# Kernel optimization log

Hardware: AMD Instinct MI355X
Metric: run time of the kernel (lower is better)

The kernel has to match this reference:

```python
import jax, jax.numpy as jnp
import numpy as np

NUM_HEADS = 16
THETA = 10000.0


def setup_inputs() -> dict:
    key = jax.random.key(0)
    k1, k2, k3, k4 = jax.random.split(key, 4)
    B, T, D = 2, 2048, 1024
    x = jax.random.normal(k1, (B, T, D), dtype=jnp.float32)
    token_positions = jnp.sort(
        jax.random.randint(k2, (B, T), 0, 2048), axis=-1
    ).astype(jnp.int32)
    sigma_qkv = float(np.sqrt(2.0 / (D + 3 * D)))
    sigma_out = float(np.sqrt(2.0 / (D + D)))
    W_qkv = jax.random.normal(k3, (3 * D, D), dtype=jnp.float32) * sigma_qkv
    W_out = jax.random.normal(k4, (D, D), dtype=jnp.float32) * sigma_out
    return {"x": x, "token_positions": token_positions, "W_qkv": W_qkv, "W_out": W_out}


def _apply_rope(t, cos, sin):
    # t: [B, H, T, d_k]; cos/sin: [B, T, d_k//2]
    B, H, T, dk = t.shape
    t2 = t.reshape(B, H, T, dk // 2, 2)
    te, to = t2[..., 0], t2[..., 1]
    c = cos[:, None]  # [B, 1, T, dk//2]
    s = sin[:, None]
    ye = te * c - to * s
    yo = to * c + te * s
    return jnp.stack([ye, yo], axis=-1).reshape(B, H, T, dk)


def reference(x, token_positions, W_qkv, W_out):
    B, T, D = x.shape
    H = NUM_HEADS
    dk = D // H

    # fused QKV projection: [B, T, 3D] -> split (three, h, d) on last dim
    qkv = jnp.einsum("btd,od->bto", x, W_qkv).reshape(B, T, 3, H, dk)
    qkv = jnp.transpose(qkv, (2, 0, 3, 1, 4))  # [3, B, H, T, dk]
    q, k, v = qkv[0], qkv[1], qkv[2]

    # RoPE angles from token positions
    n = jnp.arange(dk // 2, dtype=jnp.float32)
    inv_freq = THETA ** (-2.0 * n / dk)  # [dk//2]
    angles = token_positions.astype(jnp.float32)[..., None] * inv_freq  # [B, T, dk//2]
    cos, sin = jnp.cos(angles), jnp.sin(angles)
    q = _apply_rope(q, cos, sin)
    k = _apply_rope(k, cos, sin)

    # causal scaled dot-product attention
    scores = jnp.einsum("bhid,bhjd->bhij", q, k) / jnp.sqrt(jnp.float32(dk))
    causal = jnp.tril(jnp.ones((T, T), dtype=bool))
    scores = jnp.where(causal, scores, -jnp.inf)
    probs = jax.nn.softmax(scores, axis=-1)
    attn = jnp.einsum("bhij,bhjd->bhid", probs, v)  # [B, H, T, dk]

    concat = jnp.transpose(attn, (0, 2, 1, 3)).reshape(B, T, D)
    return jnp.einsum("btd,od->bto", concat, W_out)
```

## Files before the change

kernel.cpp:

```cpp
#include <hip/hip_runtime.h>
#include <hip/hip_bf16.h>
#include <cmath>

#define T_SEQ 2048
#define D_MODEL 1024
#define NHEAD 16
#define DK 64

typedef short bf16x8 __attribute__((ext_vector_type(8)));
typedef float f32x4 __attribute__((ext_vector_type(4)));
typedef float f32x16 __attribute__((ext_vector_type(16)));
typedef unsigned uint2v __attribute__((ext_vector_type(2)));

union U8 { unsigned u[4]; bf16x8 v; };

#define VMCNT(n) asm volatile("s_waitcnt vmcnt(" #n ")" ::: "memory")
#define BAR() __builtin_amdgcn_s_barrier()
#define SFENCE() __builtin_amdgcn_sched_barrier(0)

__device__ __forceinline__ short f2b(float f) {
    unsigned u = __builtin_bit_cast(unsigned, f);
    unsigned r = (u + 0x7FFFu + ((u >> 16) & 1u)) >> 16;
    return (short)r;
}

__device__ __forceinline__ void gll16(const void* g, void* l) {
    __builtin_amdgcn_global_load_lds(
        (__attribute__((address_space(1))) void*)g,
        (__attribute__((address_space(3))) void*)l, 16, 0, 0);
}

__device__ __forceinline__ bf16x8 lds_frag(const short* base, int row, int chunk) {
    return *reinterpret_cast<const bf16x8*>(
        (const char*)base + row * 128 + ((chunk * 16) ^ ((row & 7) << 4)));
}

__device__ __forceinline__ unsigned pkbf16(float a, float b) {
    unsigned r;
    asm("v_cvt_pk_bf16_f32 %0, %1, %2" : "=v"(r) : "v"(a), "v"(b));
    return r;
}
__device__ __forceinline__ void pl32swap(unsigned& a, unsigned& b) {
    uint2v r = __builtin_amdgcn_permlane32_swap(a, b, false, false);
    a = r.x; b = r.y;
}

__global__ __launch_bounds__(256) void cvt_all(const float* __restrict__ x,
                                               const float* __restrict__ wq,
                                               const float* __restrict__ wo,
                                               const int* __restrict__ pos,
                                               short* __restrict__ xb,
                                               short* __restrict__ wqb,
                                               short* __restrict__ wob,
                                               float* __restrict__ ct,
                                               float* __restrict__ st) {
    int i = blockIdx.x * 256 + threadIdx.x;
    if (i >= 1048576) {
        int j = i - 1048576;
        int bt = j >> 5, n = j & 31;
        float p = (float)pos[bt];
        float invf = expf((float)n * (-2.0f / (float)DK) * 9.210340371976184f);
        float s, c;
        sincosf(p * invf, &s, &c);
        ct[j] = c; st[j] = s;
        return;
    }
    const float* src;
    short* dst;
    int srcoff, c;
    if (i < 524288) {
        c = i;
        int tile = c >> 9, cc = c & 511;
        int kblk = cc >> 7, row = cc & 127;
        int rb = tile >> 5, kb = tile & 31;
        srcoff = (rb * 128 + row) * D_MODEL + kb * 32 + kblk * 8;
        src = x; dst = xb;
    } else if (i < 917504) {
        c = i - 524288;
        int tile = c >> 9, cc = c & 511;
        int kblk = cc >> 7, row = cc & 127;
        int rb = tile >> 5, kb = tile & 31;
        srcoff = (rb * 128 + row) * D_MODEL + kb * 32 + kblk * 8;
        src = wq; dst = wqb;
    } else {
        c = i - 917504;
        int tile = c >> 8, cc = c & 255;
        int kblk = cc >> 6, row = cc & 63;
        int nb = tile >> 5, kb = tile & 31;
        srcoff = (nb * 64 + row) * D_MODEL + kb * 32 + kblk * 8;
        src = wo; dst = wob;
    }
    float4 a = *reinterpret_cast<const float4*>(src + srcoff);
    float4 b = *reinterpret_cast<const float4*>(src + srcoff + 4);
    bf16x8 v;
    v[0] = f2b(a.x); v[1] = f2b(a.y); v[2] = f2b(a.z); v[3] = f2b(a.w);
    v[4] = f2b(b.x); v[5] = f2b(b.y); v[6] = f2b(b.z); v[7] = f2b(b.w);
    reinterpret_cast<bf16x8*>(dst)[c] = v;
}

__global__ __launch_bounds__(256, 3) void gemm_qkv(const short* __restrict__ xb,
                                                   const short* __restrict__ wb,
                                                   const float* __restrict__ ct,
                                                   const float* __restrict__ st,
                                                   short* __restrict__ Qo,
                                                   short* __restrict__ Ko,
                                                   short* __restrict__ Vt) {
    __shared__ short SM[3][8192];
    const int tid = threadIdx.x;
    const int w = tid >> 6, l = tid & 63, lg = l >> 4, li = l & 15;
    const int wr = w >> 1, wc = w & 1;
    const int bn = blockIdx.x * 128, bm = blockIdx.y * 128;

    const short* pA = xb + (size_t)blockIdx.y * 32 * 4096 + (w * 128 + l) * 8;
    const short* pB = wb + (size_t)blockIdx.x * 32 * 4096 + (w * 128 + l) * 8;

    f32x4 zero = {0.f, 0.f, 0.f, 0.f};
    f32x4 acc[4][4];
#pragma unroll
    for (int m = 0; m < 4; ++m)
#pragma unroll
        for (int n = 0; n < 4; ++n) acc[m][n] = zero;

#define GSTAGE(buf, t_)                                               \
    do {                                                              \
        const size_t ko = (size_t)(t_) * 4096;                        \
        gll16(pA + ko,       &SM[buf][w * 1024]);                     \
        gll16(pA + ko + 512, &SM[buf][w * 1024 + 512]);               \
        gll16(pB + ko,       &SM[buf][4096 + w * 1024]);              \
        gll16(pB + ko + 512, &SM[buf][4096 + w * 1024 + 512]);        \
    } while (0)

    GSTAGE(0, 0);
    GSTAGE(1, 1);

    for (int t = 0; t < 32; ++t) {
        if (t < 31) { VMCNT(4); } else { VMCNT(0); }
        BAR();
        SFENCE();
        if (t + 2 < 32) GSTAGE((t + 2) % 3, t + 2);
        const short* Ac = &SM[t % 3][0];
        const short* Bc = &SM[t % 3][4096];
        bf16x8 a[4], b[4];
#pragma unroll
        for (int m = 0; m < 4; ++m)
            a[m] = *reinterpret_cast<const bf16x8*>(&Ac[lg * 1024 + (wr * 64 + m * 16 + li) * 8]);
#pragma unroll
        for (int n = 0; n < 4; ++n)
            b[n] = *reinterpret_cast<const bf16x8*>(&Bc[lg * 1024 + (wc * 64 + n * 16 + li) * 8]);
        __builtin_amdgcn_s_setprio(1);
#pragma unroll
        for (int m = 0; m < 4; ++m)
#pragma unroll
            for (int n = 0; n < 4; ++n)
                acc[m][n] = __builtin_amdgcn_mfma_f32_16x16x32_bf16(a[m], b[n], acc[m][n], 0, 0, 0);
        __builtin_amdgcn_s_setprio(0);
    }
#undef GSTAGE

    const int which = bn >> 10;
    const int h = ((bn >> 6) + wc) & 15;
    if (which == 2) {
        __syncthreads();
        short* scr = &SM[0][0] + w * 4096;
#pragma unroll
        for (int n = 0; n < 4; ++n)
#pragma unroll
            for (int m = 0; m < 4; ++m)
#pragma unroll
                for (int rp = 0; rp < 2; ++rp) {
                    int d = n * 16 + li;
                    int t64 = m * 16 + lg * 4 + rp * 2;
                    unsigned pk = pkbf16(acc[m][n][rp * 2], acc[m][n][rp * 2 + 1]);
                    *reinterpret_cast<unsigned*>(
                        (char*)scr + ((d * 128 + t64 * 2) ^ ((d & 7) << 4))) = pk;
                }
        const int mi0 = bm + wr * 64;
        const int b0 = mi0 >> 11, t0 = mi0 & (T_SEQ - 1);
        short* vbase = Vt + (size_t)(b0 * NHEAD + h) * DK * T_SEQ + t0;
#pragma unroll
        for (int db = 0; db < 8; ++db) {
            int d = db * 8 + (l >> 3);
            int ch = l & 7;
            bf16x8 v = *reinterpret_cast<const bf16x8*>(
                (char*)scr + ((d * 128 + ch * 16) ^ ((d & 7) << 4)));
            *reinterpret_cast<bf16x8*>(vbase + (size_t)d * T_SEQ + ch * 8) = v;
        }
    } else {
#pragma unroll
        for (int n = 0; n < 4; ++n) {
            const int d = n * 16 + li;
#pragma unroll
            for (int m = 0; m < 4; ++m)
#pragma unroll
                for (int r = 0; r < 4; ++r) {
                    const int mi = bm + wr * 64 + m * 16 + lg * 4 + r;
                    const int b_ = mi >> 11, tt = mi & (T_SEQ - 1);
                    float v = acc[m][n][r];
                    float vp = __shfl_xor(v, 1);
                    int nn = n * 8 + (li >> 1);
                    float c = ct[(size_t)mi * 32 + nn];
                    float s = st[(size_t)mi * 32 + nn];
                    float o = (d & 1) ? (v * c + vp * s) : (v * c - vp * s);
                    if (which == 0) o *= 0.18033688011112042f;
                    short* dst = (which == 0) ? Qo : Ko;
                    dst[((size_t)((b_ * NHEAD + h) * T_SEQ + tt)) * DK + d] = f2b(o);
                }
        }
    }
}

__global__ __launch_bounds__(128, 2) void attn(const short* __restrict__ Q,
                                               const short* __restrict__ K,
                                               const short* __restrict__ Vt,
                                               short* __restrict__ Cc) {
    __shared__ short Kls[2][4096];
    __shared__ short Vls[2][4096];

    const int bid = blockIdx.x;
    const int bh = bid & 31;
    const int qt = 31 - (bid >> 5);
    const int ntb = qt + 1;

    const int tid = threadIdx.x;
    const int w = tid >> 6, l = tid & 63;
    const int l31 = l & 31, hi = l >> 5, hi4 = hi * 4, hi8 = hi * 8;
    const int q0w = qt * 64 + w * 32;

    const short* Qh = Q + (size_t)bh * T_SEQ * DK;
    const short* Kh = K + (size_t)bh * T_SEQ * DK;
    const short* Vh = Vt + (size_t)bh * DK * T_SEQ;

    bf16x8 qf[4];
#pragma unroll
    for (int ks = 0; ks < 4; ++ks)
        qf[ks] = *reinterpret_cast<const bf16x8*>(&Qh[(size_t)(q0w + l31) * DK + ks * 16 + hi8]);

    f32x16 o0 = {0.f,0.f,0.f,0.f,0.f,0.f,0.f,0.f,0.f,0.f,0.f,0.f,0.f,0.f,0.f,0.f};
    f32x16 o1 = o0;
    float m = -3.0e38f;
    float lsum = 0.f;

    int rr[4], cb[4];
#pragma unroll
    for (int j = 0; j < 4; ++j) {
        int c = j * 128 + tid;
        rr[j] = c >> 3;
        cb[j] = ((c & 7) ^ (rr[j] & 7)) * 8;
    }

    auto astage = [&](int buf, int n0_) {
#pragma unroll
        for (int j = 0; j < 4; ++j)
            gll16(Kh + (size_t)(n0_ + rr[j]) * DK + cb[j], &Kls[buf][j * 1024 + w * 512]);
#pragma unroll
        for (int j = 0; j < 4; ++j)
            gll16(Vh + (size_t)rr[j] * T_SEQ + n0_ + cb[j], &Vls[buf][j * 1024 + w * 512]);
    };

    astage(0, 0);

    for (int t = 0; t < ntb; ++t) {
        VMCNT(0);
        BAR();
        SFENCE();
        if (t + 1 < ntb) astage((t + 1) & 1, (t + 1) * 64);
        const int n0 = t * 64;
        const short* Kc = Kls[t & 1];
        const short* Vc = Vls[t & 1];

        f32x16 s0 = {0.f,0.f,0.f,0.f,0.f,0.f,0.f,0.f,0.f,0.f,0.f,0.f,0.f,0.f,0.f,0.f};
        f32x16 s1 = s0;
        __builtin_amdgcn_s_setprio(1);
#pragma unroll
        for (int ks = 0; ks < 4; ++ks) {
            bf16x8 kf0 = lds_frag(Kc, l31,      ks * 2 + hi);
            bf16x8 kf1 = lds_frag(Kc, 32 + l31, ks * 2 + hi);
            s0 = __builtin_amdgcn_mfma_f32_32x32x16_bf16(kf0, qf[ks], s0, 0, 0, 0);
            s1 = __builtin_amdgcn_mfma_f32_32x32x16_bf16(kf1, qf[ks], s1, 0, 0, 0);
        }
        __builtin_amdgcn_s_setprio(0);

        float p[32];
#pragma unroll
        for (int r = 0; r < 16; ++r) { p[r] = s0[r]; p[16 + r] = s1[r]; }

        if (n0 + 64 > q0w) {
            const int qrel = q0w + l31 - n0;
#pragma unroll
            for (int r = 0; r < 16; ++r) {
                const int kvm = (r & 3) + 8 * (r >> 2) + hi4;
                if (kvm > qrel) p[r] = -3.0e38f;
                if (kvm + 32 > qrel) p[16 + r] = -3.0e38f;
            }
        }

        float t16[16];
#pragma unroll
        for (int r = 0; r < 16; ++r) t16[r] = fmaxf(p[r], p[16 + r]);
#pragma unroll
        for (int d = 8; d >= 1; d >>= 1)
#pragma unroll
            for (int r = 0; r < 8; ++r)
                if (r < d) t16[r] = fmaxf(t16[r], t16[r + d]);
        float tmax = fmaxf(t16[0], __shfl_xor(t16[0], 32));

        if (__any(tmax > m + 8.0f)) {
            float mnew = fmaxf(m, tmax);
            float alpha = __builtin_amdgcn_exp2f(m - mnew);
            m = mnew;
#pragma unroll
            for (int r = 0; r < 16; ++r) {
                float ar = __shfl(alpha, (r & 3) + 8 * (r >> 2) + hi4);
                o0[r] *= ar; o1[r] *= ar;
            }
            lsum *= alpha;
        }

#pragma unroll
        for (int r = 0; r < 32; ++r) p[r] = __builtin_amdgcn_exp2f(p[r] - m);
        float a16[16];
#pragma unroll
        for (int r = 0; r < 16; ++r) a16[r] = p[r] + p[16 + r];
#pragma unroll
        for (int d = 8; d >= 1; d >>= 1)
#pragma unroll
            for (int r = 0; r < 8; ++r)
                if (r < d) a16[r] += a16[r + d];
        lsum += a16[0] + __shfl_xor(a16[0], 32);

        __builtin_amdgcn_s_setprio(1);
#pragma unroll
        for (int kb = 0; kb < 2; ++kb) {
            unsigned pk0 = pkbf16(p[kb * 16 + 0],  p[kb * 16 + 1]);
            unsigned pk1 = pkbf16(p[kb * 16 + 2],  p[kb * 16 + 3]);
            unsigned pk2 = pkbf16(p[kb * 16 + 4],  p[kb * 16 + 5]);
            unsigned pk3 = pkbf16(p[kb * 16 + 6],  p[kb * 16 + 7]);
            unsigned pk4 = pkbf16(p[kb * 16 + 8],  p[kb * 16 + 9]);
            unsigned pk5 = pkbf16(p[kb * 16 + 10], p[kb * 16 + 11]);
            unsigned pk6 = pkbf16(p[kb * 16 + 12], p[kb * 16 + 13]);
            unsigned pk7 = pkbf16(p[kb * 16 + 14], p[kb * 16 + 15]);
            pl32swap(pk0, pk2); pl32swap(pk1, pk3);
            pl32swap(pk4, pk6); pl32swap(pk5, pk7);
            U8 f0, f1;
            f0.u[0] = pk0; f0.u[1] = pk1; f0.u[2] = pk2; f0.u[3] = pk3;
            f1.u[0] = pk4; f1.u[1] = pk5; f1.u[2] = pk6; f1.u[3] = pk7;
            bf16x8 v00 = lds_frag(Vc, l31,      kb * 4 + hi);
            bf16x8 v01 = lds_frag(Vc, l31,      kb * 4 + 2 + hi);
            bf16x8 v10 = lds_frag(Vc, 32 + l31, kb * 4 + hi);
            bf16x8 v11 = lds_frag(Vc, 32 + l31, kb * 4 + 2 + hi);
            o0 = __builtin_amdgcn_mfma_f32_32x32x16_bf16(f0.v, v00, o0, 0, 0, 0);
            o0 = __builtin_amdgcn_mfma_f32_32x32x16_bf16(f1.v, v01, o0, 0, 0, 0);
            o1 = __builtin_amdgcn_mfma_f32_32x32x16_bf16(f0.v, v10, o1, 0, 0, 0);
            o1 = __builtin_amdgcn_mfma_f32_32x32x16_bf16(f1.v, v11, o1, 0, 0, 0);
        }
        __builtin_amdgcn_s_setprio(0);
    }

    const int b = bh >> 4, h = bh & 15;
    const float linv = 1.0f / lsum;
#pragma unroll
    for (int r = 0; r < 16; ++r) {
        const int qoff = (r & 3) + 8 * (r >> 2) + hi4;
        float inv = __shfl(linv, qoff);
        const int mg = b * T_SEQ + q0w + qoff;
        const int mb = mg >> 7, row = mg & 127;
        const int kblk = l31 >> 3, el = l & 7;
        Cc[((size_t)(mb * 32 + h * 2 + 0)) * 4096 + kblk * 1024 + row * 8 + el] = f2b(o0[r] * inv);
        Cc[((size_t)(mb * 32 + h * 2 + 1)) * 4096 + kblk * 1024 + row * 8 + el] = f2b(o1[r] * inv);
    }
}

__global__ __launch_bounds__(256, 3) void gemm_out(const short* __restrict__ ab,
                                                   const short* __restrict__ wb,
                                                   float* __restrict__ out) {
    __shared__ short SM[3][6144];
    const int tid = threadIdx.x;
    const int w = tid >> 6, l = tid & 63, lg = l >> 4, li = l & 15;
    const int wr = w >> 1, wc = w & 1;
    const int bn = blockIdx.x * 64, bm = blockIdx.y * 128;

    const short* pA = ab + (size_t)blockIdx.y * 32 * 4096 + (w * 128 + l) * 8;
    const short* pB = wb + (size_t)blockIdx.x * 32 * 2048 + (w * 64 + l) * 8;

    f32x4 zero = {0.f, 0.f, 0.f, 0.f};
    f32x4 acc[4][2];
#pragma unroll
    for (int m = 0; m < 4; ++m)
#pragma unroll
        for (int n = 0; n < 2; ++n) acc[m][n] = zero;

#define OSTAGE(buf, t_)                                                  \
    do {                                                                 \
        gll16(pA + (size_t)(t_) * 4096,       &SM[buf][w * 1024]);       \
        gll16(pA + (size_t)(t_) * 4096 + 512, &SM[buf][w * 1024 + 512]); \
        gll16(pB + (size_t)(t_) * 2048,       &SM[buf][4096 + w * 512]); \
    } while (0)

    OSTAGE(0, 0);
    OSTAGE(1, 1);

    for (int t = 0; t < 32; ++t) {
        if (t < 31) { VMCNT(3); } else { VMCNT(0); }
        BAR();
        SFENCE();
        if (t + 2 < 32) OSTAGE((t + 2) % 3, t + 2);
        const short* Ac = &SM[t % 3][0];
        const short* Bc = &SM[t % 3][4096];
        bf16x8 a[4], b[2];
#pragma unroll
        for (int m = 0; m < 4; ++m)
            a[m] = *reinterpret_cast<const bf16x8*>(&Ac[lg * 1024 + (wr * 64 + m * 16 + li) * 8]);
#pragma unroll
        for (int n = 0; n < 2; ++n)
            b[n] = *reinterpret_cast<const bf16x8*>(&Bc[lg * 512 + (wc * 32 + n * 16 + li) * 8]);
        __builtin_amdgcn_s_setprio(1);
#pragma unroll
        for (int m = 0; m < 4; ++m)
#pragma unroll
            for (int n = 0; n < 2; ++n)
                acc[m][n] = __builtin_amdgcn_mfma_f32_16x16x32_bf16(a[m], b[n], acc[m][n], 0, 0, 0);
        __builtin_amdgcn_s_setprio(0);
    }
#undef OSTAGE

#pragma unroll
    for (int m = 0; m < 4; ++m)
#pragma unroll
        for (int n = 0; n < 2; ++n)
#pragma unroll
            for (int r = 0; r < 4; ++r) {
                const int mi = bm + wr * 64 + m * 16 + lg * 4 + r;
                out[(size_t)mi * D_MODEL + bn + wc * 32 + n * 16 + li] = acc[m][n][r];
            }
}

extern "C" void kernel_launch(void* const* d_in, const int* in_sizes, int n_in,
                              void* d_out, int out_size, void* d_ws, size_t ws_size,
                              hipStream_t stream) {
    const float* x    = (const float*)d_in[0];
    const int*   pos  = (const int*)d_in[1];
    const float* wqkv = (const float*)d_in[2];
    const float* wout = (const float*)d_in[3];
    float* out = (float*)d_out;

    char* ws = (char*)d_ws;
    size_t off = 0;
    short* xb  = (short*)(ws + off); off += (size_t)4096 * 1024 * 2;
    short* wqb = (short*)(ws + off); off += (size_t)3072 * 1024 * 2;
    short* wob = (short*)(ws + off); off += (size_t)1024 * 1024 * 2;
    short* Q   = (short*)(ws + off); off += (size_t)32 * 2048 * 64 * 2;
    short* Kb  = (short*)(ws + off); off += (size_t)32 * 2048 * 64 * 2;
    short* Vt  = (short*)(ws + off); off += (size_t)32 * 64 * 2048 * 2;
    off += 4096;
    short* Cc  = (short*)(ws + off); off += (size_t)4096 * 1024 * 2;
    float* ct  = (float*)(ws + off); off += (size_t)4096 * 32 * 4;
    float* st  = (float*)(ws + off); off += (size_t)4096 * 32 * 4;

    cvt_all<<<4608, 256, 0, stream>>>(x, wqkv, wout, pos, xb, wqb, wob, ct, st);
    gemm_qkv<<<dim3(24, 32), 256, 0, stream>>>(xb, wqb, ct, st, Q, Kb, Vt);
    attn<<<1024, 128, 0, stream>>>(Q, Kb, Vt, Cc);
    gemm_out<<<dim3(16, 32), 256, 0, stream>>>(Cc, wob, out);
}
```

Baseline: 115.2 us.

## Load V fragments directly from global into registers, drop V LDS buffer

V^T fragments for the PV MFMA are now read straight from global memory into registers at the start of each tile, instead of being staged through a double-buffered LDS array. This halves LDS use so the launch bound can be raised to three blocks per SM, and it removes the LDS reads for V. In exchange, each wave issues uncached-style global loads whose latency now falls on the critical path. The loads are waited on at the next iteration's vmcnt(0) together with the K prefetch, and register pressure rises under the tighter launch bound.

After: 127.3 us. +10.5%, slower.

```diff
diff --git a/kernel.cpp b/kernel.cpp
--- a/kernel.cpp
+++ b/kernel.cpp
@@ -209,12 +209,11 @@
     }
 }
 
-__global__ __launch_bounds__(128, 2) void attn(const short* __restrict__ Q,
+__global__ __launch_bounds__(128, 3) void attn(const short* __restrict__ Q,
                                                const short* __restrict__ K,
                                                const short* __restrict__ Vt,
                                                short* __restrict__ Cc) {
     __shared__ short Kls[2][4096];
-    __shared__ short Vls[2][4096];
 
     const int bid = blockIdx.x;
     const int bh = bid & 31;
@@ -247,26 +246,35 @@
         rr[j] = c >> 3;
         cb[j] = ((c & 7) ^ (rr[j] & 7)) * 8;
     }
-
-    auto astage = [&](int buf, int n0_) {
+    auto kstage = [&](int buf, int n0_) {
 #pragma unroll
         for (int j = 0; j < 4; ++j)
             gll16(Kh + (size_t)(n0_ + rr[j]) * DK + cb[j], &Kls[buf][j * 1024 + w * 512]);
-#pragma unroll
-        for (int j = 0; j < 4; ++j)
-            gll16(Vh + (size_t)rr[j] * T_SEQ + n0_ + cb[j], &Vls[buf][j * 1024 + w * 512]);
     };
 
-    astage(0, 0);
+    const short* vrow0 = Vh + (size_t)l31 * T_SEQ;
+    const short* vrow1 = Vh + (size_t)(32 + l31) * T_SEQ;
+
+    kstage(0, 0);
 
     for (int t = 0; t < ntb; ++t) {
         VMCNT(0);
         BAR();
+        const int n0 = t * 64;
+
+        bf16x8 v00[2], v01[2], v10[2], v11[2];
+#pragma unroll
+        for (int kb = 0; kb < 2; ++kb) {
+            const int co = n0 + (kb * 4 + hi) * 8;
+            v00[kb] = *reinterpret_cast<const bf16x8*>(vrow0 + co);
+            v01[kb] = *reinterpret_cast<const bf16x8*>(vrow0 + co + 16);
+            v10[kb] = *reinterpret_cast<const bf16x8*>(vrow1 + co);
+            v11[kb] = *reinterpret_cast<const bf16x8*>(vrow1 + co + 16);
+        }
+        if (t + 1 < ntb) kstage((t + 1) & 1, (t + 1) * 64);
         SFENCE();
-        if (t + 1 < ntb) astage((t + 1) & 1, (t + 1) * 64);
-        const int n0 = t * 64;
+
         const short* Kc = Kls[t & 1];
-        const short* Vc = Vls[t & 1];
 
         f32x16 s0 = {0.f,0.f,0.f,0.f,0.f,0.f,0.f,0.f,0.f,0.f,0.f,0.f,0.f,0.f,0.f,0.f};
         f32x16 s1 = s0;
@@ -344,14 +352,10 @@
             U8 f0, f1;
             f0.u[0] = pk0; f0.u[1] = pk1; f0.u[2] = pk2; f0.u[3] = pk3;
             f1.u[0] = pk4; f1.u[1] = pk5; f1.u[2] = pk6; f1.u[3] = pk7;
-            bf16x8 v00 = lds_frag(Vc, l31,      kb * 4 + hi);
-            bf16x8 v01 = lds_frag(Vc, l31,      kb * 4 + 2 + hi);
-            bf16x8 v10 = lds_frag(Vc, 32 + l31, kb * 4 + hi);
-            bf16x8 v11 = lds_frag(Vc, 32 + l31, kb * 4 + 2 + hi);
-            o0 = __builtin_amdgcn_mfma_f32_32x32x16_bf16(f0.v, v00, o0, 0, 0, 0);
-            o0 = __builtin_amdgcn_mfma_f32_32x32x16_bf16(f1.v, v01, o0, 0, 0, 0);
-            o1 = __builtin_amdgcn_mfma_f32_32x32x16_bf16(f0.v, v10, o1, 0, 0, 0);
-            o1 = __builtin_amdgcn_mfma_f32_32x32x16_bf16(f1.v, v11, o1, 0, 0, 0);
+            o0 = __builtin_amdgcn_mfma_f32_32x32x16_bf16(f0.v, v00[kb], o0, 0, 0, 0);
+            o0 = __builtin_amdgcn_mfma_f32_32x32x16_bf16(f1.v, v01[kb], o0, 0, 0, 0);
+            o1 = __builtin_amdgcn_mfma_f32_32x32x16_bf16(f0.v, v10[kb], o1, 0, 0, 0);
+            o1 = __builtin_amdgcn_mfma_f32_32x32x16_bf16(f1.v, v11[kb], o1, 0, 0, 0);
         }
         __builtin_amdgcn_s_setprio(0);
     }
```
